# Kernel tuning notes

Measured on AMD Instinct MI355X. Metric: run time of the kernel, lower is better.

The kernel has to match this reference:

```python
import jax, jax.numpy as jnp
import numpy as np

N_NODES = 100000


def setup_inputs() -> dict:
    key = jax.random.key(0)
    k1, k2, k3 = jax.random.split(key, 3)
    x = jax.random.normal(k1, (100000, 64), dtype=jnp.float32)
    edge_index = jax.random.randint(k2, (2, 1000000), 0, 100000, dtype=jnp.int64)
    edge_attr = jax.random.uniform(k3, (1000000, 64), dtype=jnp.float32)
    return {"x": x, "edge_index": edge_index, "edge_attr": edge_attr}


def reference(x, edge_index, edge_attr):
    # gather source node features [E, d], weight by edge_attr, scatter-add to dest
    msg = x[edge_index[1]] * edge_attr  # [E, d]
    out = jax.ops.segment_sum(msg, edge_index[0], num_segments=N_NODES)  # [N, d]
    return out
```

## Files before the change

kernel.cpp:

```cpp
#include <hip/hip_runtime.h>
#include <hip/hip_bf16.h>


#define SCAN_BLOCK 256
#define ELEMS_PER_THREAD 16
#define SCAN_CHUNK (SCAN_BLOCK * ELEMS_PER_THREAD)

__global__ void hist_kernel(const int* __restrict__ edge_index,
                            int* __restrict__ counts, int E) {
    int i = blockIdx.x * blockDim.x + threadIdx.x;
    int e = i * 4;
    if (e + 3 < E) {
        int4 d = *(const int4*)(edge_index + e);
        atomicAdd(&counts[d.x], 1);
        atomicAdd(&counts[d.y], 1);
        atomicAdd(&counts[d.z], 1);
        atomicAdd(&counts[d.w], 1);
    } else {
        for (; e < E; e++) atomicAdd(&counts[edge_index[e]], 1);
    }
}

__global__ void scan_block_kernel(const int* __restrict__ counts,
                                  int* __restrict__ local_scan,
                                  int* __restrict__ block_sums, int N) {
    __shared__ int buf[SCAN_BLOCK];
    const int t = threadIdx.x;
    const int base = blockIdx.x * SCAN_CHUNK + t * ELEMS_PER_THREAD;
    int v[ELEMS_PER_THREAD];
    int s = 0;
#pragma unroll
    for (int k = 0; k < ELEMS_PER_THREAD; k++) {
        int i = base + k;
        v[k] = (i < N) ? counts[i] : 0;
        s += v[k];
    }
    buf[t] = s;
    __syncthreads();
    for (int off = 1; off < SCAN_BLOCK; off <<= 1) {
        int add = (t >= off) ? buf[t - off] : 0;
        __syncthreads();
        buf[t] += add;
        __syncthreads();
    }
    int excl = buf[t] - s;
#pragma unroll
    for (int k = 0; k < ELEMS_PER_THREAD; k++) {
        int i = base + k;
        if (i < N) local_scan[i] = excl;
        excl += v[k];
    }
    if (t == SCAN_BLOCK - 1) block_sums[blockIdx.x] = buf[t];
}

__global__ void scan_sums_kernel(const int* __restrict__ block_sums,
                                 int* __restrict__ block_prefix, int nb) {
    if (threadIdx.x == 0 && blockIdx.x == 0) {
        int acc = 0;
        for (int i = 0; i < nb; i++) { block_prefix[i] = acc; acc += block_sums[i]; }
        block_prefix[nb] = acc;
    }
}

__global__ void scan_add_kernel(const int* __restrict__ local_scan,
                                const int* __restrict__ block_prefix,
                                int* __restrict__ offsets,
                                int* __restrict__ cursor, int N, int nb) {
    int i = blockIdx.x * blockDim.x + threadIdx.x;
    if (i < N) {
        int v = local_scan[i] + block_prefix[i / SCAN_CHUNK];
        offsets[i] = v;
        cursor[i] = v;
    }
    if (i == 0) offsets[N] = block_prefix[nb];
}

__global__ void place_kernel(const int* __restrict__ edge_index,
                             int* __restrict__ cursor,
                             uint2* __restrict__ perm, int E) {
    int i = blockIdx.x * blockDim.x + threadIdx.x;
    int e = i * 2;
    if (e + 1 < E) {
        int2 d = *(const int2*)(edge_index + e);
        int2 s = *(const int2*)(edge_index + E + e);
        int p0 = atomicAdd(&cursor[d.x], 1);
        perm[p0] = make_uint2((unsigned)e, (unsigned)s.x);
        int p1 = atomicAdd(&cursor[d.y], 1);
        perm[p1] = make_uint2((unsigned)(e + 1), (unsigned)s.y);
    } else if (e < E) {
        int d = edge_index[e], s = edge_index[E + e];
        perm[atomicAdd(&cursor[d], 1)] = make_uint2((unsigned)e, (unsigned)s);
    }
}

__global__ void gather_kernel(const float* __restrict__ x,
                              const float* __restrict__ edge_attr,
                              const int* __restrict__ offsets,
                              const uint2* __restrict__ perm,
                              float* __restrict__ out, int N) {
    long long tid = (long long)blockIdx.x * blockDim.x + threadIdx.x;
    int n = (int)(tid >> 4);
    int c = ((int)tid & 15) << 2;
    if (n >= N) return;
    int p = offsets[n];
    const int end = offsets[n + 1];
    float4 acc = make_float4(0.f, 0.f, 0.f, 0.f);
    for (; p + 1 < end; p += 2) {
        uint2 es0 = perm[p];
        uint2 es1 = perm[p + 1];
        const float4 ea0 = *(const float4*)(edge_attr + (size_t)es0.x * 64 + c);
        const float4 xv0 = *(const float4*)(x + (size_t)es0.y * 64 + c);
        const float4 ea1 = *(const float4*)(edge_attr + (size_t)es1.x * 64 + c);
        const float4 xv1 = *(const float4*)(x + (size_t)es1.y * 64 + c);
        acc.x += ea0.x * xv0.x + ea1.x * xv1.x;
        acc.y += ea0.y * xv0.y + ea1.y * xv1.y;
        acc.z += ea0.z * xv0.z + ea1.z * xv1.z;
        acc.w += ea0.w * xv0.w + ea1.w * xv1.w;
    }
    if (p < end) {
        uint2 es = perm[p];
        const float4 ea = *(const float4*)(edge_attr + (size_t)es.x * 64 + c);
        const float4 xv = *(const float4*)(x + (size_t)es.y * 64 + c);
        acc.x += ea.x * xv.x;
        acc.y += ea.y * xv.y;
        acc.z += ea.z * xv.z;
        acc.w += ea.w * xv.w;
    }
    *(float4*)(out + (size_t)n * 64 + c) = acc;
}

extern "C" void kernel_launch(void* const* d_in, const int* in_sizes, int n_in,
                              void* d_out, int out_size, void* d_ws, size_t ws_size,
                              hipStream_t stream) {
    const float* x          = (const float*)d_in[0];
    const int*   edge_index = (const int*)d_in[1];
    const float* edge_attr  = (const float*)d_in[2];
    float*       out        = (float*)d_out;

    const int E = in_sizes[1] / 2;
    const int N = out_size / 64;
    const int nb = (N + SCAN_CHUNK - 1) / SCAN_CHUNK;

    auto align256 = [](size_t v) { return (v + 255) & ~(size_t)255; };
    char* w = (char*)d_ws;
    size_t off = 0;
    int* offsets      = (int*)(w + off); off = align256(off + (size_t)(N + 1) * 4);
    int* cursor       = (int*)(w + off); off = align256(off + (size_t)N * 4);
    int* counts       = (int*)(w + off); off = align256(off + (size_t)N * 4);
    int* local_scan   = (int*)(w + off); off = align256(off + (size_t)N * 4);
    int* block_sums   = (int*)(w + off); off = align256(off + (size_t)(nb + 1) * 4);
    int* block_prefix = (int*)(w + off); off = align256(off + (size_t)(nb + 1) * 4);
    uint2* perm       = (uint2*)(w + off);

    hipMemsetAsync(counts, 0, (size_t)N * 4, stream);

    const int block = 256;
    hist_kernel<<<(E / 4 + block) / block + 1, block, 0, stream>>>(edge_index, counts, E);
    scan_block_kernel<<<nb, SCAN_BLOCK, 0, stream>>>(counts, local_scan, block_sums, N);
    scan_sums_kernel<<<1, 64, 0, stream>>>(block_sums, block_prefix, nb);
    scan_add_kernel<<<(N + block - 1) / block, block, 0, stream>>>(
        local_scan, block_prefix, offsets, cursor, N, nb);
    place_kernel<<<(E / 2 + block - 1) / block + 1, block, 0, stream>>>(
        edge_index, cursor, perm, E);

    const long long gthreads = (long long)N * 16;
    gather_kernel<<<(int)((gthreads + block - 1) / block), block, 0, stream>>>(
        x, edge_attr, offsets, perm, out, N);
}
```

Measured before the change: 503.4 us.

## Use one wavefront per node in gather, fold block-prefix scan into scan_add

The gather kernel now assigns a full 64-lane wavefront to each destination node. Four 16-lane groups each handle every fourth edge, and the partial sums are combined with cross-lane shuffles. perm and edge_attr are read with nontemporal loads to keep the reused x rows in cache. The single-thread scan_sums kernel is removed, and each scan_add block now sums its own preceding block_sums, which cuts one launch. The cost is more threads per node, so low-degree nodes (about 10 edges on average) leave lanes idle, plus a shuffle reduction per node.

```diff
diff --git a/kernel.cpp b/kernel.cpp
--- a/kernel.cpp
+++ b/kernel.cpp
@@ -5,6 +5,9 @@
 #define SCAN_BLOCK 256
 #define ELEMS_PER_THREAD 16
 #define SCAN_CHUNK (SCAN_BLOCK * ELEMS_PER_THREAD)
+
+typedef float  vfloat4 __attribute__((ext_vector_type(4)));
+typedef unsigned int vuint2 __attribute__((ext_vector_type(2)));
 
 __global__ void hist_kernel(const int* __restrict__ edge_index,
                             int* __restrict__ counts, int E) {
@@ -53,80 +56,78 @@
     if (t == SCAN_BLOCK - 1) block_sums[blockIdx.x] = buf[t];
 }
 
-__global__ void scan_sums_kernel(const int* __restrict__ block_sums,
-                                 int* __restrict__ block_prefix, int nb) {
-    if (threadIdx.x == 0 && blockIdx.x == 0) {
-        int acc = 0;
-        for (int i = 0; i < nb; i++) { block_prefix[i] = acc; acc += block_sums[i]; }
-        block_prefix[nb] = acc;
-    }
-}
-
 __global__ void scan_add_kernel(const int* __restrict__ local_scan,
-                                const int* __restrict__ block_prefix,
+                                const int* __restrict__ block_sums,
                                 int* __restrict__ offsets,
                                 int* __restrict__ cursor, int N, int nb) {
+    __shared__ int prefix_s;
+    const int chunk = (blockIdx.x * SCAN_BLOCK) / SCAN_CHUNK;
+    if (threadIdx.x == 0) {
+        int acc = 0;
+        for (int j = 0; j < chunk; j++) acc += block_sums[j];
+        prefix_s = acc;
+        if (blockIdx.x == 0) {
+            int tot = 0;
+            for (int j = 0; j < nb; j++) tot += block_sums[j];
+            offsets[N] = tot;
+        }
+    }
+    __syncthreads();
     int i = blockIdx.x * blockDim.x + threadIdx.x;
     if (i < N) {
-        int v = local_scan[i] + block_prefix[i / SCAN_CHUNK];
+        int v = local_scan[i] + prefix_s;
         offsets[i] = v;
         cursor[i] = v;
     }
-    if (i == 0) offsets[N] = block_prefix[nb];
 }
 
 __global__ void place_kernel(const int* __restrict__ edge_index,
                              int* __restrict__ cursor,
-                             uint2* __restrict__ perm, int E) {
+                             vuint2* __restrict__ perm, int E) {
     int i = blockIdx.x * blockDim.x + threadIdx.x;
     int e = i * 2;
     if (e + 1 < E) {
         int2 d = *(const int2*)(edge_index + e);
         int2 s = *(const int2*)(edge_index + E + e);
         int p0 = atomicAdd(&cursor[d.x], 1);
-        perm[p0] = make_uint2((unsigned)e, (unsigned)s.x);
+        perm[p0] = (vuint2){(unsigned)e, (unsigned)s.x};
         int p1 = atomicAdd(&cursor[d.y], 1);
-        perm[p1] = make_uint2((unsigned)(e + 1), (unsigned)s.y);
+        perm[p1] = (vuint2){(unsigned)(e + 1), (unsigned)s.y};
     } else if (e < E) {
         int d = edge_index[e], s = edge_index[E + e];
-        perm[atomicAdd(&cursor[d], 1)] = make_uint2((unsigned)e, (unsigned)s);
+        perm[atomicAdd(&cursor[d], 1)] = (vuint2){(unsigned)e, (unsigned)s};
     }
 }
 
 __global__ void gather_kernel(const float* __restrict__ x,
                               const float* __restrict__ edge_attr,
                               const int* __restrict__ offsets,
-                              const uint2* __restrict__ perm,
+                              const vuint2* __restrict__ perm,
                               float* __restrict__ out, int N) {
-    long long tid = (long long)blockIdx.x * blockDim.x + threadIdx.x;
-    int n = (int)(tid >> 4);
-    int c = ((int)tid & 15) << 2;
+    const int lane = threadIdx.x & 63;
+    const int n = blockIdx.x * (blockDim.x >> 6) + (threadIdx.x >> 6);
     if (n >= N) return;
-    int p = offsets[n];
-    const int end = offsets[n + 1];
-    float4 acc = make_float4(0.f, 0.f, 0.f, 0.f);
-    for (; p + 1 < end; p += 2) {
-        uint2 es0 = perm[p];
-        uint2 es1 = perm[p + 1];
-        const float4 ea0 = *(const float4*)(edge_attr + (size_t)es0.x * 64 + c);
-        const float4 xv0 = *(const float4*)(x + (size_t)es0.y * 64 + c);
-        const float4 ea1 = *(const float4*)(edge_attr + (size_t)es1.x * 64 + c);
-        const float4 xv1 = *(const float4*)(x + (size_t)es1.y * 64 + c);
-        acc.x += ea0.x * xv0.x + ea1.x * xv1.x;
-        acc.y += ea0.y * xv0.y + ea1.y * xv1.y;
-        acc.z += ea0.z * xv0.z + ea1.z * xv1.z;
-        acc.w += ea0.w * xv0.w + ea1.w * xv1.w;
+    const int g = lane >> 4;
+    const int c = (lane & 15) << 2;
+    const int start = offsets[n];
+    const int end   = offsets[n + 1];
+    vfloat4 acc = {0.f, 0.f, 0.f, 0.f};
+    for (int p = start + g; p < end; p += 4) {
+        vuint2 es = __builtin_nontemporal_load(&perm[p]);
+        vfloat4 ea = __builtin_nontemporal_load(
+            (const vfloat4*)(edge_attr + (size_t)es.x * 64 + c));
+        vfloat4 xv = *(const vfloat4*)(x + (size_t)es.y * 64 + c);
+        acc += ea * xv;
     }
-    if (p < end) {
-        uint2 es = perm[p];
-        const float4 ea = *(const float4*)(edge_attr + (size_t)es.x * 64 + c);
-        const float4 xv = *(const float4*)(x + (size_t)es.y * 64 + c);
-        acc.x += ea.x * xv.x;
-        acc.y += ea.y * xv.y;
-        acc.z += ea.z * xv.z;
-        acc.w += ea.w * xv.w;
-    }
-    *(float4*)(out + (size_t)n * 64 + c) = acc;
+    acc.x += __shfl_xor(acc.x, 16, 64);
+    acc.y += __shfl_xor(acc.y, 16, 64);
+    acc.z += __shfl_xor(acc.z, 16, 64);
+    acc.w += __shfl_xor(acc.w, 16, 64);
+    acc.x += __shfl_xor(acc.x, 32, 64);
+    acc.y += __shfl_xor(acc.y, 32, 64);
+    acc.z += __shfl_xor(acc.z, 32, 64);
+    acc.w += __shfl_xor(acc.w, 32, 64);
+    if (g == 0) *(vfloat4*)(out + (size_t)n * 64 + c) = acc;
 }
 
 extern "C" void kernel_launch(void* const* d_in, const int* in_sizes, int n_in,
@@ -144,26 +145,25 @@
     auto align256 = [](size_t v) { return (v + 255) & ~(size_t)255; };
     char* w = (char*)d_ws;
     size_t off = 0;
-    int* offsets      = (int*)(w + off); off = align256(off + (size_t)(N + 1) * 4);
-    int* cursor       = (int*)(w + off); off = align256(off + (size_t)N * 4);
-    int* counts       = (int*)(w + off); off = align256(off + (size_t)N * 4);
-    int* local_scan   = (int*)(w + off); off = align256(off + (size_t)N * 4);
-    int* block_sums   = (int*)(w + off); off = align256(off + (size_t)(nb + 1) * 4);
-    int* block_prefix = (int*)(w + off); off = align256(off + (size_t)(nb + 1) * 4);
-    uint2* perm       = (uint2*)(w + off);
+    int* offsets    = (int*)(w + off); off = align256(off + (size_t)(N + 1) * 4);
+    int* cursor     = (int*)(w + off); off = align256(off + (size_t)N * 4);
+    int* counts     = (int*)(w + off); off = align256(off + (size_t)N * 4);
+    int* local_scan = (int*)(w + off); off = align256(off + (size_t)N * 4);
+    int* block_sums = (int*)(w + off); off = align256(off + (size_t)(nb + 1) * 4);
+    vuint2* perm    = (vuint2*)(w + off);
 
     hipMemsetAsync(counts, 0, (size_t)N * 4, stream);
 
     const int block = 256;
-    hist_kernel<<<(E / 4 + block) / block + 1, block, 0, stream>>>(edge_index, counts, E);
+    const int hist_grid = ((E + 3) / 4 + block - 1) / block;
+    hist_kernel<<<hist_grid, block, 0, stream>>>(edge_index, counts, E);
     scan_block_kernel<<<nb, SCAN_BLOCK, 0, stream>>>(counts, local_scan, block_sums, N);
-    scan_sums_kernel<<<1, 64, 0, stream>>>(block_sums, block_prefix, nb);
     scan_add_kernel<<<(N + block - 1) / block, block, 0, stream>>>(
-        local_scan, block_prefix, offsets, cursor, N, nb);
-    place_kernel<<<(E / 2 + block - 1) / block + 1, block, 0, stream>>>(
-        edge_index, cursor, perm, E);
+        local_scan, block_sums, offsets, cursor, N, nb);
+    const int place_grid = ((E + 1) / 2 + block - 1) / block;
+    place_kernel<<<place_grid, block, 0, stream>>>(edge_index, cursor, perm, E);
 
-    const long long gthreads = (long long)N * 16;
-    gather_kernel<<<(int)((gthreads + block - 1) / block), block, 0, stream>>>(
+    const int waves_per_block = block / 64;
+    gather_kernel<<<(N + waves_per_block - 1) / waves_per_block, block, 0, stream>>>(
         x, edge_attr, offsets, perm, out, N);
 }
```

Result: no change. 500.5 us (-0.6%).
